# Kernel optimization log

Hardware: AMD Instinct MI355X
Metric: run time of the kernel (lower is better)

The kernel has to match this reference:

```python
import jax, jax.numpy as jnp
import numpy as np

N, E = 50000, 800000
IN_DIM, NH = 256, 64          # in_dim, num_hidden
HID = 2 * NH                  # per-head out of GAT layers = num_hidden*2 = 128
HEADS, C = 2, 32              # heads[0]=heads[1]=2, final head=1, num_classes=32
NEG = 0.2                     # leaky relu negative slope


def _gat(h, W, al, ar, b, src, dst, heads, out, identity_res=False, res_W=None, act=None):
    # DGL-style GATConv: linear -> per-head attn logits -> edge softmax over dst -> scatter sum
    n = h.shape[0]
    feat = (h @ W).reshape(n, heads, out)              # [N, H, D]
    el = (feat * al).sum(-1)                           # [N, H]
    er = (feat * ar).sum(-1)                           # [N, H]
    e = el[src] + er[dst]                              # [E, H]
    e = jnp.where(e > 0, e, NEG * e)                   # leaky relu
    emax = jax.ops.segment_max(e, dst, num_segments=n)
    ex = jnp.exp(e - emax[dst])
    den = jax.ops.segment_sum(ex, dst, num_segments=n)
    alpha = ex / den[dst]                              # edge softmax per dst
    msg = feat[src] * alpha[..., None]                 # [E, H, D]
    rst = jax.ops.segment_sum(msg, dst, num_segments=n)  # [N, H, D]
    if identity_res:
        rst = rst + h.reshape(n, heads, out)
    elif res_W is not None:
        rst = rst + (h @ res_W).reshape(n, heads, out)
    rst = rst + b.reshape(1, heads, out)
    return act(rst) if act is not None else rst


def setup_inputs() -> dict:
    key = jax.random.key(0)
    ks = jax.random.split(key, 24)
    g = lambda i, shp, s: jax.random.normal(ks[i], shp, jnp.float32) * s
    d = {
        'inputs': g(0, (N, IN_DIM), 1.0),
        'z': g(1, (NH,), 1.0),
        'src': jax.random.randint(ks[2], (E,), 0, N, jnp.int32),
        'dst': jax.random.randint(ks[3], (E,), 0, N, jnp.int32),
        # x_to_h
        'Wx': g(4, (IN_DIM, NH), 0.06), 'bx': jnp.zeros((NH,), jnp.float32),
        # GAT layer 0: in 2*NH=128 -> heads=2, out=128
        'W0': g(5, (HID, HEADS * HID), 0.09), 'al0': g(6, (HEADS, HID), 0.09),
        'ar0': g(7, (HEADS, HID), 0.09), 'b0': jnp.zeros((HEADS * HID,), jnp.float32),
        # GAT layer 1: in 256 -> heads=2, out=128 (identity residual)
        'W1': g(8, (HEADS * HID, HEADS * HID), 0.06), 'al1': g(9, (HEADS, HID), 0.09),
        'ar1': g(10, (HEADS, HID), 0.09), 'b1': jnp.zeros((HEADS * HID,), jnp.float32),
        # final GAT: in 256 -> 1 head, out=num_classes=32, linear residual
        'Wf': g(11, (HEADS * HID, C), 0.06), 'alf': g(12, (1, C), 0.18),
        'arf': g(13, (1, C), 0.18), 'bf': jnp.zeros((C,), jnp.float32),
        'resWf': g(14, (HEADS * HID, C), 0.06),
    }
    return d


def reference(inputs, z, src, dst, Wx, bx, W0, al0, ar0, b0, W1, al1, ar1, b1, Wf, alf, arf, bf, resWf):
    n = inputs.shape[0]
    h = jax.nn.relu(inputs @ Wx + bx)                          # [N, NH]
    h = jnp.concatenate([h, jnp.broadcast_to(z, (n, z.shape[0]))], axis=1)  # [N, 2*NH]
    h = h / (jnp.linalg.norm(h, axis=1, keepdims=True) + 1e-6)
    h = _gat(h, W0, al0, ar0, b0, src, dst, HEADS, HID, act=jax.nn.elu).reshape(n, -1)
    h = _gat(h, W1, al1, ar1, b1, src, dst, HEADS, HID, identity_res=True, act=jax.nn.elu).reshape(n, -1)
    logits = _gat(h, Wf, alf, arf, bf, src, dst, 1, C, res_W=resWf).mean(1)  # [N, C]
    return logits
```

## Files before the change

kernel.cpp:

```cpp
#include <hip/hip_runtime.h>
#include <hip/hip_bf16.h>
#include <math.h>

#define N_NODES 50000
#define N_EDGES 800000
#define NEG 0.2f

typedef __attribute__((ext_vector_type(4))) float f32x4;
typedef __attribute__((ext_vector_type(8))) short bf16x8;

__device__ __forceinline__ float bf2f(ushort u) {
    union { uint i; float f; } t; t.i = ((uint)u) << 16; return t.f;
}
__device__ __forceinline__ ushort f2bf(float f) {
    union { float f; uint i; } t; t.f = f;
    uint i = t.i;
    uint r = (i + 0x7FFFu + ((i >> 16) & 1u)) >> 16;
    return (ushort)r;
}

__device__ __forceinline__ void gload16(const ushort* src, ushort* ldst) {
    __builtin_amdgcn_global_load_lds(
        (const __attribute__((address_space(1))) uint32_t*)src,
        (__attribute__((address_space(3))) uint32_t*)ldst, 16, 0, 0);
}

__global__ void k_fillp(const int* __restrict__ src, const int* __restrict__ dst,
                        int* __restrict__ cnt, int* __restrict__ esrc, int E) {
    int e = blockIdx.x * 256 + threadIdx.x;
    if (e < E) {
        int d = dst[e];
        int p = atomicAdd(&cnt[d], 1);
        if (p < 64) esrc[((size_t)d << 6) + p] = src[e];
    }
}

__global__ void k_prep2(const float* __restrict__ Wx, const float* __restrict__ W0,
                        const float* __restrict__ W1, const float* __restrict__ Wf,
                        const float* __restrict__ rWf, const float* __restrict__ inputs,
                        const float* __restrict__ z,
                        ushort* __restrict__ BtX, ushort* __restrict__ Bt0,
                        ushort* __restrict__ Bt1, ushort* __restrict__ BtF,
                        ushort* __restrict__ Ab, float* __restrict__ zW0,
                        int* __restrict__ cnt) {
    int i = blockIdx.x * 256 + threadIdx.x;
    const int base2 = 131072 + N_NODES * 32;
    const int base3 = base2 + 256;
    if (i < 16384) {
        int n = i >> 8, k = i & 255;
        BtX[i] = f2bf(Wx[k * 64 + n]);
    } else if (i < 49152) {
        int t = i - 16384;
        int n = t >> 7, k = t & 127;
        Bt0[t] = f2bf(W0[k * 256 + n]);
    } else if (i < 114688) {
        int t = i - 49152;
        int n = t >> 8, k = t & 255;
        Bt1[t] = f2bf(W1[k * 256 + n]);
    } else if (i < 131072) {
        int t = i - 114688;
        int n = t >> 8, k = t & 255;
        float v = (n < 32) ? Wf[k * 32 + n] : rWf[k * 32 + (n - 32)];
        BtF[t] = f2bf(v);
    } else if (i < base2) {
        int t = i - 131072;
        float4 v0 = ((const float4*)inputs)[2 * t];
        float4 v1 = ((const float4*)inputs)[2 * t + 1];
        ushort4 a, b;
        a.x = f2bf(v0.x); a.y = f2bf(v0.y); a.z = f2bf(v0.z); a.w = f2bf(v0.w);
        b.x = f2bf(v1.x); b.y = f2bf(v1.y); b.z = f2bf(v1.z); b.w = f2bf(v1.w);
        ((ushort4*)Ab)[2 * t]     = a;
        ((ushort4*)Ab)[2 * t + 1] = b;
    } else if (i < base3) {
        int c = i - base2;
        float s = 0.f;
        for (int k = 0; k < 64; ++k) s += z[k] * W0[(64 + k) * 256 + c];
        zW0[c] = s;
    } else if (i < base3 + N_NODES) {
        cnt[i - base3] = 0;
    }
}

__global__ __launch_bounds__(256) void k_gemmA(
    const ushort* __restrict__ Ax, const ushort* __restrict__ BtX,
    const ushort* __restrict__ Bt0, const float* __restrict__ bx,
    const float* __restrict__ zv, const float* __restrict__ zW0,
    const float* __restrict__ alv, const float* __restrict__ arv,
    ushort* __restrict__ feat, float* __restrict__ elv, float* __restrict__ erv, int M)
{
    __shared__ ushort As1[128 * 64];
    __shared__ ushort Bs1[64 * 64];
    __shared__ ushort As2[128 * 64];
    __shared__ ushort Bs2[256 * 64];
    __shared__ float  invRow[128];

    const int tid = threadIdx.x;
    const int bm = blockIdx.x * 128;
    const int lane = tid & 63;
    const int w = tid >> 6;
    const int fr = lane & 15;
    const int kg = lane >> 4;
    const int rl = lane >> 3;
    const int bl = lane & 7;

    #pragma unroll
    for (int i = w; i < 32; i += 4) {
        int r = i * 8 + rl;
        int cb = bl ^ (r & 7);
        gload16(Bt0 + (size_t)r * 128 + cb * 8, &Bs2[i * 512]);
    }

    f32x4 acc1[2][4];
    #pragma unroll
    for (int m = 0; m < 2; ++m)
        #pragma unroll
        for (int n = 0; n < 4; ++n) acc1[m][n] = (f32x4){0.f, 0.f, 0.f, 0.f};

    for (int k0 = 0; k0 < 256; k0 += 64) {
        #pragma unroll
        for (int i = w; i < 16; i += 4) {
            int r = i * 8 + rl;
            int cb = bl ^ (r & 7);
            int gr = bm + r;
            if (gr >= M) gr = 0;
            gload16(Ax + (size_t)gr * 256 + k0 + cb * 8, &As1[i * 512]);
        }
        #pragma unroll
        for (int i = w; i < 8; i += 4) {
            int r = i * 8 + rl;
            int cb = bl ^ (r & 7);
            gload16(BtX + (size_t)r * 256 + k0 + cb * 8, &Bs1[i * 512]);
        }
        __syncthreads();
        #pragma unroll
        for (int s = 0; s < 2; ++s) {
            bf16x8 a[2], b[4];
            #pragma unroll
            for (int m = 0; m < 2; ++m) {
                int row = w * 32 + m * 16 + fr;
                int blk = (s * 4 + kg) ^ (fr & 7);
                a[m] = *(const bf16x8*)&As1[row * 64 + blk * 8];
            }
            #pragma unroll
            for (int n = 0; n < 4; ++n) {
                int row = n * 16 + fr;
                int blk = (s * 4 + kg) ^ (fr & 7);
                b[n] = *(const bf16x8*)&Bs1[row * 64 + blk * 8];
            }
            #pragma unroll
            for (int m = 0; m < 2; ++m)
                #pragma unroll
                for (int n = 0; n < 4; ++n)
                    acc1[m][n] = __builtin_amdgcn_mfma_f32_16x16x32_bf16(a[m], b[n], acc1[m][n], 0, 0, 0);
        }
        __syncthreads();
    }

    {
        float zl = zv[lane];
        float zq = zl * zl;
        #pragma unroll
        for (int off = 32; off > 0; off >>= 1) zq += __shfl_xor(zq, off, 64);
        #pragma unroll
        for (int m = 0; m < 2; ++m) {
            #pragma unroll
            for (int j = 0; j < 4; ++j) {
                int row = w * 32 + m * 16 + kg * 4 + j;
                float v[4]; float ss = 0.f;
                #pragma unroll
                for (int n = 0; n < 4; ++n) {
                    float o = acc1[m][n][j] + bx[n * 16 + fr];
                    o = fmaxf(o, 0.f);
                    v[n] = o; ss += o * o;
                }
                #pragma unroll
                for (int off = 8; off > 0; off >>= 1) ss += __shfl_xor(ss, off, 64);
                float inv = 1.f / (sqrtf(ss + zq) + 1e-6f);
                if (fr == 0) invRow[row] = inv;
                #pragma unroll
                for (int n = 0; n < 4; ++n) {
                    int b = n * 2 + (fr >> 3);
                    int p = b ^ (row & 7);
                    As2[row * 64 + p * 8 + (fr & 7)] = f2bf(v[n] * inv);
                }
            }
        }
    }
    __syncthreads();

    const int wr2 = w >> 1, wc2 = w & 1;
    f32x4 acc2[4][8];
    #pragma unroll
    for (int m = 0; m < 4; ++m)
        #pragma unroll
        for (int n = 0; n < 8; ++n) acc2[m][n] = (f32x4){0.f, 0.f, 0.f, 0.f};
    #pragma unroll
    for (int s = 0; s < 2; ++s) {
        bf16x8 a[4], b[8];
        #pragma unroll
        for (int m = 0; m < 4; ++m) {
            int row = wr2 * 64 + m * 16 + fr;
            int blk = (s * 4 + kg) ^ (fr & 7);
            a[m] = *(const bf16x8*)&As2[row * 64 + blk * 8];
        }
        #pragma unroll
        for (int n = 0; n < 8; ++n) {
            int row = wc2 * 128 + n * 16 + fr;
            int blk = (s * 4 + kg) ^ (fr & 7);
            b[n] = *(const bf16x8*)&Bs2[row * 64 + blk * 8];
        }
        #pragma unroll
        for (int m = 0; m < 4; ++m)
            #pragma unroll
            for (int n = 0; n < 8; ++n)
                acc2[m][n] = __builtin_amdgcn_mfma_f32_16x16x32_bf16(a[m], b[n], acc2[m][n], 0, 0, 0);
    }

    #pragma unroll
    for (int m = 0; m < 4; ++m) {
        #pragma unroll
        for (int j = 0; j < 4; ++j) {
            int lrow = wr2 * 64 + m * 16 + kg * 4 + j;
            int row = bm + lrow;
            float invR = invRow[lrow];
            float pe = 0.f, pr = 0.f;
            if (row < M) {
                #pragma unroll
                for (int n = 0; n < 8; ++n) {
                    int col = wc2 * 128 + n * 16 + fr;
                    float o = acc2[m][n][j] + invR * zW0[col];
                    feat[(size_t)row * 256 + col] = f2bf(o);
                    pe += o * alv[col];
                    pr += o * arv[col];
                }
            }
            #pragma unroll
            for (int off = 8; off > 0; off >>= 1) {
                pe += __shfl_xor(pe, off, 64);
                pr += __shfl_xor(pr, off, 64);
            }
            if (row < M && fr == 0) {
                elv[(size_t)row * 2 + wc2] = pe;
                erv[(size_t)row * 2 + wc2] = pr;
            }
        }
    }
}

__global__ __launch_bounds__(256) void k_gemmB(
    const ushort* __restrict__ A, const ushort* __restrict__ Bt,
    ushort* __restrict__ feat, const float* __restrict__ alv, const float* __restrict__ arv,
    float* __restrict__ elv, float* __restrict__ erv, int M)
{
    __shared__ ushort As[128 * 64];
    __shared__ ushort Bs[256 * 64];

    const int tid = threadIdx.x;
    const int bm = blockIdx.x * 128;
    const int lane = tid & 63;
    const int w = tid >> 6;
    const int wr = w >> 1, wc = w & 1;
    const int fr = lane & 15;
    const int kg = lane >> 4;
    const int rl = lane >> 3;
    const int bl = lane & 7;

    f32x4 acc[4][8];
    #pragma unroll
    for (int m = 0; m < 4; ++m)
        #pragma unroll
        for (int n = 0; n < 8; ++n) acc[m][n] = (f32x4){0.f, 0.f, 0.f, 0.f};

    for (int k0 = 0; k0 < 256; k0 += 64) {
        #pragma unroll
        for (int i = w; i < 16; i += 4) {
            int r = i * 8 + rl;
            int cb = bl ^ (r & 7);
            int gr = bm + r;
            if (gr >= M) gr = 0;
            gload16(A + (size_t)gr * 256 + k0 + cb * 8, &As[i * 512]);
        }
        #pragma unroll
        for (int i = w; i < 32; i += 4) {
            int r = i * 8 + rl;
            int cb = bl ^ (r & 7);
            gload16(Bt + (size_t)r * 256 + k0 + cb * 8, &Bs[i * 512]);
        }
        __syncthreads();
        #pragma unroll
        for (int s = 0; s < 2; ++s) {
            bf16x8 a[4], b[8];
            #pragma unroll
            for (int m = 0; m < 4; ++m) {
                int row = wr * 64 + m * 16 + fr;
                int blk = (s * 4 + kg) ^ (fr & 7);
                a[m] = *(const bf16x8*)&As[row * 64 + blk * 8];
            }
            #pragma unroll
            for (int n = 0; n < 8; ++n) {
                int row = wc * 128 + n * 16 + fr;
                int blk = (s * 4 + kg) ^ (fr & 7);
                b[n] = *(const bf16x8*)&Bs[row * 64 + blk * 8];
            }
            #pragma unroll
            for (int m = 0; m < 4; ++m)
                #pragma unroll
                for (int n = 0; n < 8; ++n)
                    acc[m][n] = __builtin_amdgcn_mfma_f32_16x16x32_bf16(a[m], b[n], acc[m][n], 0, 0, 0);
        }
        __syncthreads();
    }

    #pragma unroll
    for (int m = 0; m < 4; ++m) {
        #pragma unroll
        for (int j = 0; j < 4; ++j) {
            int row = bm + wr * 64 + m * 16 + kg * 4 + j;
            float pe = 0.f, pr = 0.f;
            if (row < M) {
                #pragma unroll
                for (int n = 0; n < 8; ++n) {
                    int col = wc * 128 + n * 16 + fr;
                    float o = acc[m][n][j];
                    feat[(size_t)row * 256 + col] = f2bf(o);
                    pe += o * alv[col];
                    pr += o * arv[col];
                }
            }
            #pragma unroll
            for (int off = 8; off > 0; off >>= 1) {
                pe += __shfl_xor(pe, off, 64);
                pr += __shfl_xor(pr, off, 64);
            }
            if (row < M && fr == 0) {
                elv[(size_t)row * 2 + wc] = pe;
                erv[(size_t)row * 2 + wc] = pr;
            }
        }
    }
}

__global__ __launch_bounds__(256) void k_gemmC(
    const ushort* __restrict__ A, const ushort* __restrict__ Bt,
    ushort* __restrict__ pkb, float* __restrict__ C2,
    const float* __restrict__ alv, const float* __restrict__ arv,
    float* __restrict__ elv, float* __restrict__ erv, int M)
{
    __shared__ ushort As[128 * 64];
    __shared__ ushort Bs[64 * 64];

    const int tid = threadIdx.x;
    const int bm = blockIdx.x * 128;
    const int lane = tid & 63;
    const int w = tid >> 6;
    const int fr = lane & 15;
    const int kg = lane >> 4;
    const int rl = lane >> 3;
    const int bl = lane & 7;

    f32x4 acc[2][4];
    #pragma unroll
    for (int m = 0; m < 2; ++m)
        #pragma unroll
        for (int n = 0; n < 4; ++n) acc[m][n] = (f32x4){0.f, 0.f, 0.f, 0.f};

    for (int k0 = 0; k0 < 256; k0 += 64) {
        #pragma unroll
        for (int i = w; i < 16; i += 4) {
            int r = i * 8 + rl;
            int cb = bl ^ (r & 7);
            int gr = bm + r;
            if (gr >= M) gr = 0;
            gload16(A + (size_t)gr * 256 + k0 + cb * 8, &As[i * 512]);
        }
        #pragma unroll
        for (int i = w; i < 8; i += 4) {
            int r = i * 8 + rl;
            int cb = bl ^ (r & 7);
            gload16(Bt + (size_t)r * 256 + k0 + cb * 8, &Bs[i * 512]);
        }
        __syncthreads();
        #pragma unroll
        for (int s = 0; s < 2; ++s) {
            bf16x8 a[2], b[4];
            #pragma unroll
            for (int m = 0; m < 2; ++m) {
                int row = w * 32 + m * 16 + fr;
                int blk = (s * 4 + kg) ^ (fr & 7);
                a[m] = *(const bf16x8*)&As[row * 64 + blk * 8];
            }
            #pragma unroll
            for (int n = 0; n < 4; ++n) {
                int row = n * 16 + fr;
                int blk = (s * 4 + kg) ^ (fr & 7);
                b[n] = *(const bf16x8*)&Bs[row * 64 + blk * 8];
            }
            #pragma unroll
            for (int m = 0; m < 2; ++m)
                #pragma unroll
                for (int n = 0; n < 4; ++n)
                    acc[m][n] = __builtin_amdgcn_mfma_f32_16x16x32_bf16(a[m], b[n], acc[m][n], 0, 0, 0);
        }
        __syncthreads();
    }

    #pragma unroll
    for (int m = 0; m < 2; ++m) {
        #pragma unroll
        for (int j = 0; j < 4; ++j) {
            int row = bm + w * 32 + m * 16 + kg * 4 + j;
            float pe = 0.f, pr = 0.f;
            if (row < M) {
                #pragma unroll
                for (int n = 0; n < 4; ++n) {
                    int col = n * 16 + fr;
                    float o = acc[m][n][j];
                    pkb[(size_t)row * 64 + col] = f2bf(o);
                    if (n >= 2) {
                        C2[(size_t)row * 32 + (col - 32)] = o;
                    } else {
                        pe += o * alv[col];
                        pr += o * arv[col];
                    }
                }
            }
            #pragma unroll
            for (int off = 8; off > 0; off >>= 1) {
                pe += __shfl_xor(pe, off, 64);
                pr += __shfl_xor(pr, off, 64);
            }
            if (row < M && fr == 0) { elv[row] = pe; erv[row] = pr; }
        }
    }
}

template<int RES>
__global__ __launch_bounds__(256) void k_edge256(
    const ushort* __restrict__ feat, const float* __restrict__ el, const float* __restrict__ er,
    const float* __restrict__ bias, const int* __restrict__ cnt, const int* __restrict__ esrc,
    ushort* __restrict__ outp, const ushort* __restrict__ resid, int n)
{
    int wid = (blockIdx.x * blockDim.x + threadIdx.x) >> 6;
    int lane = threadIdx.x & 63;
    if (wid >= n) return;
    int m = lane & 31;
    int head = lane >> 5;
    int deg = cnt[wid]; if (deg > 64) deg = 64;
    int rs = wid << 6, re = rs + deg;
    float ern = er[((size_t)wid << 1) + head];
    const char* featc = (const char*)feat;
    uint loff = (uint)lane << 3;

    float den[4] = {0.f, 0.f, 0.f, 0.f};
    f32x4 av[4];
    #pragma unroll
    for (int u = 0; u < 4; ++u) av[u] = (f32x4){0.f, 0.f, 0.f, 0.f};

    for (int c = rs; c < re; c += 32) {
        int nj = re - c; if (nj > 32) nj = 32;
        int sv = 0; float wv = 0.f;
        if (m < nj) {
            sv = esrc[c + m];
            float x = el[((uint)sv << 1) + head] + ern;
            x = (x > 0.f) ? x : NEG * x;
            wv = __expf(fminf(x, 60.f));
        }
        int j = 0;
        for (; j + 3 < nj; j += 4) {
            #pragma unroll
            for (int u = 0; u < 4; ++u) {
                int   sU = __shfl(sv, j + u, 32);
                float wU = __shfl(wv, j + u, 32);
                ushort4 vU = *(const ushort4*)(featc + (((uint)sU << 9) | loff));
                den[u] += wU;
                av[u].x += wU * bf2f(vU.x);
                av[u].y += wU * bf2f(vU.y);
                av[u].z += wU * bf2f(vU.z);
                av[u].w += wU * bf2f(vU.w);
            }
        }
        for (; j < nj; ++j) {
            int   sU = __shfl(sv, j, 32);
            float wU = __shfl(wv, j, 32);
            ushort4 vU = *(const ushort4*)(featc + (((uint)sU << 9) | loff));
            den[0] += wU;
            av[0].x += wU * bf2f(vU.x);
            av[0].y += wU * bf2f(vU.y);
            av[0].z += wU * bf2f(vU.z);
            av[0].w += wU * bf2f(vU.w);
        }
    }
    float denT = (den[0] + den[1]) + (den[2] + den[3]);
    float ax = (av[0].x + av[1].x) + (av[2].x + av[3].x);
    float ay = (av[0].y + av[1].y) + (av[2].y + av[3].y);
    float az = (av[0].z + av[1].z) + (av[2].z + av[3].z);
    float aw = (av[0].w + av[1].w) + (av[2].w + av[3].w);
    float inv = (deg > 0) ? 1.f / denT : 0.f;

    int c0i = lane * 4;
    float4 bv = *(const float4*)(bias + c0i);
    float rx = 0.f, ry = 0.f, rz = 0.f, rw = 0.f;
    if (RES) {
        ushort4 rv = ((const ushort4*)resid)[(size_t)wid * 64 + lane];
        rx = bf2f(rv.x); ry = bf2f(rv.y); rz = bf2f(rv.z); rw = bf2f(rv.w);
    }
    float ox = ax * inv + bv.x + rx;
    float oy = ay * inv + bv.y + ry;
    float oz = az * inv + bv.z + rz;
    float ow = aw * inv + bv.w + rw;
    ox = (ox > 0.f) ? ox : expm1f(ox);
    oy = (oy > 0.f) ? oy : expm1f(oy);
    oz = (oz > 0.f) ? oz : expm1f(oz);
    ow = (ow > 0.f) ? ow : expm1f(ow);
    ushort4 o;
    o.x = f2bf(ox); o.y = f2bf(oy); o.z = f2bf(oz); o.w = f2bf(ow);
    ((ushort4*)outp)[(size_t)wid * 64 + lane] = o;
}

__global__ __launch_bounds__(256) void k_edgef(
    const ushort* __restrict__ pkb, const float* __restrict__ residf,
    const float* __restrict__ elf, const float* __restrict__ erf,
    const float* __restrict__ bfv, const int* __restrict__ cnt, const int* __restrict__ esrc,
    float* __restrict__ outp, int n)
{
    int t = blockIdx.x * 256 + threadIdx.x;
    int node = t >> 4;
    int m = t & 15;
    if (node >= n) return;
    int deg = cnt[node]; if (deg > 64) deg = 64;
    int rs = node << 6, re = rs + deg;
    float ern = erf[node];
    const char* pc = (const char*)pkb;
    uint moff = (uint)m << 2;

    float den[4] = {0.f, 0.f, 0.f, 0.f};
    float a0[4] = {0.f, 0.f, 0.f, 0.f};
    float a1[4] = {0.f, 0.f, 0.f, 0.f};

    for (int c = rs; c < re; c += 16) {
        int nj = re - c; if (nj > 16) nj = 16;
        int sv = 0; float wv = 0.f;
        if (m < nj) {
            sv = esrc[c + m];
            float x = elf[sv] + ern;
            x = (x > 0.f) ? x : NEG * x;
            wv = __expf(fminf(x, 60.f));
        }
        int j = 0;
        for (; j + 3 < nj; j += 4) {
            #pragma unroll
            for (int u = 0; u < 4; ++u) {
                int   sU = __shfl(sv, j + u, 16);
                float wU = __shfl(wv, j + u, 16);
                ushort2 vU = *(const ushort2*)(pc + (((uint)sU << 7) | moff));
                den[u] += wU;
                a0[u] += wU * bf2f(vU.x);
                a1[u] += wU * bf2f(vU.y);
            }
        }
        for (; j < nj; ++j) {
            int   sU = __shfl(sv, j, 16);
            float wU = __shfl(wv, j, 16);
            ushort2 vU = *(const ushort2*)(pc + (((uint)sU << 7) | moff));
            den[0] += wU;
            a0[0] += wU * bf2f(vU.x);
            a1[0] += wU * bf2f(vU.y);
        }
    }
    float dT = (den[0] + den[1]) + (den[2] + den[3]);
    float A0 = (a0[0] + a0[1]) + (a0[2] + a0[3]);
    float A1 = (a1[0] + a1[1]) + (a1[2] + a1[3]);
    float inv = (deg > 0) ? 1.f / dT : 0.f;

    float2 rv = *(const float2*)(residf + (size_t)node * 32 + 2 * m);
    float2 bv = *(const float2*)(bfv + 2 * m);
    float2 o;
    o.x = A0 * inv + rv.x + bv.x;
    o.y = A1 * inv + rv.y + bv.y;
    *(float2*)(outp + (size_t)node * 32 + 2 * m) = o;
}

extern "C" void kernel_launch(void* const* d_in, const int* in_sizes, int n_in,
                              void* d_out, int out_size, void* d_ws, size_t ws_size,
                              hipStream_t stream) {
    const float* inputs = (const float*)d_in[0];
    const float* z      = (const float*)d_in[1];
    const int*   src    = (const int*)d_in[2];
    const int*   dst    = (const int*)d_in[3];
    const float* Wx  = (const float*)d_in[4];
    const float* bx  = (const float*)d_in[5];
    const float* W0  = (const float*)d_in[6];
    const float* al0 = (const float*)d_in[7];
    const float* ar0 = (const float*)d_in[8];
    const float* b0  = (const float*)d_in[9];
    const float* W1  = (const float*)d_in[10];
    const float* al1 = (const float*)d_in[11];
    const float* ar1 = (const float*)d_in[12];
    const float* b1  = (const float*)d_in[13];
    const float* Wf  = (const float*)d_in[14];
    const float* alf = (const float*)d_in[15];
    const float* arf = (const float*)d_in[16];
    const float* bf  = (const float*)d_in[17];
    const float* rWf = (const float*)d_in[18];
    float* out = (float*)d_out;

    const int N = N_NODES, E = N_EDGES;

    char* w = (char*)d_ws;
    auto alloc = [&](size_t bytes) -> char* {
        char* p = w;
        w += (bytes + 255) & ~(size_t)255;
        return p;
    };
    ushort* Ab    = (ushort*)alloc((size_t)N * 256 * 2);
    ushort* feat  = (ushort*)alloc((size_t)N * 256 * 2);
    ushort* h1    = (ushort*)alloc((size_t)N * 256 * 2);
    ushort* h2    = (ushort*)alloc((size_t)N * 256 * 2);
    ushort* pkb   = (ushort*)alloc((size_t)N * 64 * 2);
    float*  residf= (float*)alloc((size_t)N * 32 * 4);
    float*  elerb = (float*)alloc((size_t)N * 4 * 4);
    float*  elb   = elerb;
    float*  erb   = elerb + (size_t)N * 2;
    ushort* BtX   = (ushort*)alloc((size_t)64 * 256 * 2);
    ushort* Bt0   = (ushort*)alloc((size_t)256 * 128 * 2);
    ushort* Bt1   = (ushort*)alloc((size_t)256 * 256 * 2);
    ushort* BtF   = (ushort*)alloc((size_t)64 * 256 * 2);
    float*  zW0   = (float*)alloc(256 * 4);
    int* cnt  = (int*)alloc((size_t)N * 4);
    int* esrc = (int*)alloc((size_t)N * 64 * 4);

    int prep_threads = 131072 + N * 32 + 256 + N;
    k_prep2<<<(prep_threads + 255) / 256, 256, 0, stream>>>(Wx, W0, W1, Wf, rWf, inputs, z,
                                                            BtX, Bt0, Bt1, BtF, Ab, zW0, cnt);
    k_fillp<<<(E + 255) / 256, 256, 0, stream>>>(src, dst, cnt, esrc, E);

    int nwb = (N + 3) / 4;
    int ngb = (N + 127) / 128;

    k_gemmA<<<ngb, 256, 0, stream>>>(Ab, BtX, Bt0, bx, z, zW0, al0, ar0, feat, elb, erb, N);
    k_edge256<0><<<nwb, 256, 0, stream>>>(feat, elb, erb, b0, cnt, esrc, h1, nullptr, N);

    k_gemmB<<<ngb, 256, 0, stream>>>(h1, Bt1, feat, al1, ar1, elb, erb, N);
    k_edge256<1><<<nwb, 256, 0, stream>>>(feat, elb, erb, b1, cnt, esrc, h2, h1, N);

    k_gemmC<<<ngb, 256, 0, stream>>>(h2, BtF, pkb, residf, alf, arf, elb, erb, N);
    k_edgef<<<(N + 15) / 16, 256, 0, stream>>>(pkb, residf, elb, erb, bf, cnt, esrc, out, N);
}
```

Baseline: 271.4 us.

## Fuse fp32-to-bf16 input conversion into first GEMM and stage edge weights in LDS

The separate prep pass that converted the 50000x256 fp32 input to bf16 is removed. k_gemmA now reads fp32 rows directly, packs them with v_cvt_pk_bf16_f32 and writes the swizzled tile into LDS, which saves a full write and re-read of the bf16 copy. The edge aggregation kernels also replace per-edge cross-lane shuffles of source index and weight with an int2 buffer in LDS that is read back by broadcast. The A-tile load in the GEMM becomes a synchronous register load instead of the async global_load_lds path, which may add latency.

```diff
diff --git a/kernel.cpp b/kernel.cpp
--- a/kernel.cpp
+++ b/kernel.cpp
@@ -17,6 +17,11 @@
     uint i = t.i;
     uint r = (i + 0x7FFFu + ((i >> 16) & 1u)) >> 16;
     return (ushort)r;
+}
+__device__ __forceinline__ uint cvtpk(float lo, float hi) {
+    uint r;
+    asm("v_cvt_pk_bf16_f32 %0, %1, %2" : "=v"(r) : "v"(lo), "v"(hi));
+    return r;
 }
 
 __device__ __forceinline__ void gload16(const ushort* src, ushort* ldst) {
@@ -37,15 +42,12 @@
 
 __global__ void k_prep2(const float* __restrict__ Wx, const float* __restrict__ W0,
                         const float* __restrict__ W1, const float* __restrict__ Wf,
-                        const float* __restrict__ rWf, const float* __restrict__ inputs,
-                        const float* __restrict__ z,
+                        const float* __restrict__ rWf, const float* __restrict__ z,
                         ushort* __restrict__ BtX, ushort* __restrict__ Bt0,
                         ushort* __restrict__ Bt1, ushort* __restrict__ BtF,
-                        ushort* __restrict__ Ab, float* __restrict__ zW0,
-                        int* __restrict__ cnt) {
+                        float* __restrict__ zW0, int* __restrict__ cnt) {
     int i = blockIdx.x * 256 + threadIdx.x;
-    const int base2 = 131072 + N_NODES * 32;
-    const int base3 = base2 + 256;
+    const int base3 = 131072 + 256;
     if (i < 16384) {
         int n = i >> 8, k = i & 255;
         BtX[i] = f2bf(Wx[k * 64 + n]);
@@ -62,17 +64,8 @@
         int n = t >> 8, k = t & 255;
         float v = (n < 32) ? Wf[k * 32 + n] : rWf[k * 32 + (n - 32)];
         BtF[t] = f2bf(v);
-    } else if (i < base2) {
-        int t = i - 131072;
-        float4 v0 = ((const float4*)inputs)[2 * t];
-        float4 v1 = ((const float4*)inputs)[2 * t + 1];
-        ushort4 a, b;
-        a.x = f2bf(v0.x); a.y = f2bf(v0.y); a.z = f2bf(v0.z); a.w = f2bf(v0.w);
-        b.x = f2bf(v1.x); b.y = f2bf(v1.y); b.z = f2bf(v1.z); b.w = f2bf(v1.w);
-        ((ushort4*)Ab)[2 * t]     = a;
-        ((ushort4*)Ab)[2 * t + 1] = b;
     } else if (i < base3) {
-        int c = i - base2;
+        int c = i - 131072;
         float s = 0.f;
         for (int k = 0; k < 64; ++k) s += z[k] * W0[(64 + k) * 256 + c];
         zW0[c] = s;
@@ -82,7 +75,7 @@
 }
 
 __global__ __launch_bounds__(256) void k_gemmA(
-    const ushort* __restrict__ Ax, const ushort* __restrict__ BtX,
+    const float* __restrict__ Ax, const ushort* __restrict__ BtX,
     const ushort* __restrict__ Bt0, const float* __restrict__ bx,
     const float* __restrict__ zv, const float* __restrict__ zW0,
     const float* __restrict__ alv, const float* __restrict__ arv,
@@ -116,14 +109,26 @@
         #pragma unroll
         for (int n = 0; n < 4; ++n) acc1[m][n] = (f32x4){0.f, 0.f, 0.f, 0.f};
 
+    const int ar_ = tid >> 1;
+    const int ab_ = (tid & 1) * 4;
+    int agr = bm + ar_; if (agr >= M) agr = 0;
+    const float* ap0 = Ax + (size_t)agr * 256 + ab_ * 8;
+
     for (int k0 = 0; k0 < 256; k0 += 64) {
-        #pragma unroll
-        for (int i = w; i < 16; i += 4) {
-            int r = i * 8 + rl;
-            int cb = bl ^ (r & 7);
-            int gr = bm + r;
-            if (gr >= M) gr = 0;
-            gload16(Ax + (size_t)gr * 256 + k0 + cb * 8, &As1[i * 512]);
+        {
+            const float* ap = ap0 + k0;
+            #pragma unroll
+            for (int b = 0; b < 4; ++b) {
+                float4 v0 = *(const float4*)(ap + b * 8);
+                float4 v1 = *(const float4*)(ap + b * 8 + 4);
+                uint4 pk;
+                pk.x = cvtpk(v0.x, v0.y);
+                pk.y = cvtpk(v0.z, v0.w);
+                pk.z = cvtpk(v1.x, v1.y);
+                pk.w = cvtpk(v1.z, v1.w);
+                int p = (ab_ + b) ^ (ar_ & 7);
+                *(uint4*)&As1[ar_ * 64 + p * 8] = pk;
+            }
         }
         #pragma unroll
         for (int i = w; i < 8; i += 4) {
@@ -440,8 +445,10 @@
     const float* __restrict__ bias, const int* __restrict__ cnt, const int* __restrict__ esrc,
     ushort* __restrict__ outp, const ushort* __restrict__ resid, int n)
 {
+    __shared__ int2 swb[4][2][32];
     int wid = (blockIdx.x * blockDim.x + threadIdx.x) >> 6;
     int lane = threadIdx.x & 63;
+    int w = threadIdx.x >> 6;
     if (wid >= n) return;
     int m = lane & 31;
     int head = lane >> 5;
@@ -458,20 +465,21 @@
 
     for (int c = rs; c < re; c += 32) {
         int nj = re - c; if (nj > 32) nj = 32;
-        int sv = 0; float wv = 0.f;
         if (m < nj) {
-            sv = esrc[c + m];
-            float x = el[((uint)sv << 1) + head] + ern;
+            int s = esrc[c + m];
+            float x = el[((uint)s << 1) + head] + ern;
             x = (x > 0.f) ? x : NEG * x;
-            wv = __expf(fminf(x, 60.f));
+            float wv = __expf(fminf(x, 60.f));
+            int2 t; t.x = s; t.y = __float_as_int(wv);
+            swb[w][head][m] = t;
         }
         int j = 0;
         for (; j + 3 < nj; j += 4) {
             #pragma unroll
             for (int u = 0; u < 4; ++u) {
-                int   sU = __shfl(sv, j + u, 32);
-                float wU = __shfl(wv, j + u, 32);
-                ushort4 vU = *(const ushort4*)(featc + (((uint)sU << 9) | loff));
+                int2 p = swb[w][head][j + u];
+                float wU = __int_as_float(p.y);
+                ushort4 vU = *(const ushort4*)(featc + (((uint)p.x << 9) | loff));
                 den[u] += wU;
                 av[u].x += wU * bf2f(vU.x);
                 av[u].y += wU * bf2f(vU.y);
@@ -480,9 +488,9 @@
             }
         }
         for (; j < nj; ++j) {
-            int   sU = __shfl(sv, j, 32);
-            float wU = __shfl(wv, j, 32);
-            ushort4 vU = *(const ushort4*)(featc + (((uint)sU << 9) | loff));
+            int2 p = swb[w][head][j];
+            float wU = __int_as_float(p.y);
+            ushort4 vU = *(const ushort4*)(featc + (((uint)p.x << 9) | loff));
             den[0] += wU;
             av[0].x += wU * bf2f(vU.x);
             av[0].y += wU * bf2f(vU.y);
@@ -523,9 +531,11 @@
     const float* __restrict__ bfv, const int* __restrict__ cnt, const int* __restrict__ esrc,
     float* __restrict__ outp, int n)
 {
+    __shared__ int2 swf[16][16];
     int t = blockIdx.x * 256 + threadIdx.x;
     int node = t >> 4;
     int m = t & 15;
+    int nb = threadIdx.x >> 4;
     if (node >= n) return;
     int deg = cnt[node]; if (deg > 64) deg = 64;
     int rs = node << 6, re = rs + deg;
@@ -539,29 +549,30 @@
 
     for (int c = rs; c < re; c += 16) {
         int nj = re - c; if (nj > 16) nj = 16;
-        int sv = 0; float wv = 0.f;
         if (m < nj) {
-            sv = esrc[c + m];
-            float x = elf[sv] + ern;
+            int s = esrc[c + m];
+            float x = elf[s] + ern;
             x = (x > 0.f) ? x : NEG * x;
-            wv = __expf(fminf(x, 60.f));
+            float wv = __expf(fminf(x, 60.f));
+            int2 tt; tt.x = s; tt.y = __float_as_int(wv);
+            swf[nb][m] = tt;
         }
         int j = 0;
         for (; j + 3 < nj; j += 4) {
             #pragma unroll
             for (int u = 0; u < 4; ++u) {
-                int   sU = __shfl(sv, j + u, 16);
-                float wU = __shfl(wv, j + u, 16);
-                ushort2 vU = *(const ushort2*)(pc + (((uint)sU << 7) | moff));
+                int2 p = swf[nb][j + u];
+                float wU = __int_as_float(p.y);
+                ushort2 vU = *(const ushort2*)(pc + (((uint)p.x << 7) | moff));
                 den[u] += wU;
                 a0[u] += wU * bf2f(vU.x);
                 a1[u] += wU * bf2f(vU.y);
             }
         }
         for (; j < nj; ++j) {
-            int   sU = __shfl(sv, j, 16);
-            float wU = __shfl(wv, j, 16);
-            ushort2 vU = *(const ushort2*)(pc + (((uint)sU << 7) | moff));
+            int2 p = swf[nb][j];
+            float wU = __int_as_float(p.y);
+            ushort2 vU = *(const ushort2*)(pc + (((uint)p.x << 7) | moff));
             den[0] += wU;
             a0[0] += wU * bf2f(vU.x);
             a1[0] += wU * bf2f(vU.y);
@@ -612,7 +623,6 @@
         w += (bytes + 255) & ~(size_t)255;
         return p;
     };
-    ushort* Ab    = (ushort*)alloc((size_t)N * 256 * 2);
     ushort* feat  = (ushort*)alloc((size_t)N * 256 * 2);
     ushort* h1    = (ushort*)alloc((size_t)N * 256 * 2);
     ushort* h2    = (ushort*)alloc((size_t)N * 256 * 2);
@@ -629,15 +639,15 @@
     int* cnt  = (int*)alloc((size_t)N * 4);
     int* esrc = (int*)alloc((size_t)N * 64 * 4);
 
-    int prep_threads = 131072 + N * 32 + 256 + N;
-    k_prep2<<<(prep_threads + 255) / 256, 256, 0, stream>>>(Wx, W0, W1, Wf, rWf, inputs, z,
-                                                            BtX, Bt0, Bt1, BtF, Ab, zW0, cnt);
+    int prep_threads = 131072 + 256 + N;
+    k_prep2<<<(prep_threads + 255) / 256, 256, 0, stream>>>(Wx, W0, W1, Wf, rWf, z,
+                                                            BtX, Bt0, Bt1, BtF, zW0, cnt);
     k_fillp<<<(E + 255) / 256, 256, 0, stream>>>(src, dst, cnt, esrc, E);
 
     int nwb = (N + 3) / 4;
     int ngb = (N + 127) / 128;
 
-    k_gemmA<<<ngb, 256, 0, stream>>>(Ab, BtX, Bt0, bx, z, zW0, al0, ar0, feat, elb, erb, N);
+    k_gemmA<<<ngb, 256, 0, stream>>>(inputs, BtX, Bt0, bx, z, zW0, al0, ar0, feat, elb, erb, N);
     k_edge256<0><<<nwb, 256, 0, stream>>>(feat, elb, erb, b0, cnt, esrc, h1, nullptr, N);
 
     k_gemmB<<<ngb, 256, 0, stream>>>(h1, Bt1, feat, al1, ar1, elb, erb, N);
```

Result: faster. 265.2 us (median of 2 runs) (-2.3%).
